# Performance work log

Hardware: AMD Instinct MI355X
Metric: run time of the kernel (lower is better)

Reference implementation:

```python
import jax, jax.numpy as jnp
import numpy as np

N = 100000
E = 800000
HID = 128
HEADS = 4
HD = HID // HEADS  # 32
EPS_SOFTMAX = 1e-16
LN_EPS = 1e-5


def setup_inputs() -> dict:
    key = jax.random.key(0)
    ks = jax.random.split(key, 12)
    s = 1.0 / np.sqrt(HID)
    x = jax.random.normal(ks[0], (N, HID), dtype=jnp.float32)
    edge_index = jax.random.randint(ks[1], (2, E), 0, N, dtype=jnp.int64)
    Wq = jax.random.normal(ks[2], (HID, HID), dtype=jnp.float32) * s
    bq = jnp.zeros((HID,), jnp.float32)
    Wk = jax.random.normal(ks[3], (HID, HID), dtype=jnp.float32) * s
    bk = jnp.zeros((HID,), jnp.float32)
    Wv = jax.random.normal(ks[4], (HID, HID), dtype=jnp.float32) * s
    bv = jnp.zeros((HID,), jnp.float32)
    Ws = jax.random.normal(ks[5], (HID, HID), dtype=jnp.float32) * s
    bs = jnp.zeros((HID,), jnp.float32)
    gamma = jnp.ones((HID,), jnp.float32)
    beta = jnp.zeros((HID,), jnp.float32)
    return {"x": x, "edge_index": edge_index, "Wq": Wq, "bq": bq,
            "Wk": Wk, "bk": bk, "Wv": Wv, "bv": bv,
            "Ws": Ws, "bs": bs, "gamma": gamma, "beta": beta}


def _transformer_conv(x, edge_index, Wq, bq, Wk, bk, Wv, bv, Ws, bs, gamma, beta):
    src = edge_index[0]  # message source j
    dst = edge_index[1]  # message target i
    # Projections -> [N, HEADS, HD]
    q = (x @ Wq + bq).reshape(N, HEADS, HD)
    k = (x @ Wk + bk).reshape(N, HEADS, HD)
    v = (x @ Wv + bv).reshape(N, HEADS, HD)
    # Edge-wise attention logits [E, HEADS]
    alpha = jnp.einsum('ehd,ehd->eh', q[dst], k[src]) / np.sqrt(HD).astype(np.float32)
    # Segment (per-destination) softmax, numerically stable
    amax = jax.ops.segment_max(alpha, dst, num_segments=N)  # [N, HEADS]
    amax = jnp.where(jnp.isfinite(amax), amax, 0.0)
    ex = jnp.exp(alpha - amax[dst])
    denom = jax.ops.segment_sum(ex, dst, num_segments=N)
    alpha = ex / (denom[dst] + EPS_SOFTMAX)
    # Weighted scatter-add of values
    out = jax.ops.segment_sum(alpha[:, :, None] * v[src], dst, num_segments=N)
    out = out.reshape(N, HID)
    # Root/skip connection (PyG root_weight=True, concat=True)
    out = out + x @ Ws + bs
    # LayerNorm
    mu = jnp.mean(out, axis=-1, keepdims=True)
    var = jnp.mean(jnp.square(out - mu), axis=-1, keepdims=True)
    return (out - mu) * jax.lax.rsqrt(var + LN_EPS) * gamma + beta


def reference(x, edge_index, Wq, bq, Wk, bk, Wv, bv, Ws, bs, gamma, beta):
    return _transformer_conv(x, edge_index, Wq, bq, Wk, bk, Wv, bv, Ws, bs, gamma, beta)
```

## Files before the change

### kernel.cpp

```cpp
#include <hip/hip_runtime.h>
#include <math.h>

#define N_NODES 100000
#define N_EDGES 800000
#define HID 128
#define HEADS 4
#define HD 32

#define KSCALE_L2E 0.2550348554422384f

#define PROJ_BLOCKS 1563
#define FILL_BLOCKS 3125

typedef __attribute__((ext_vector_type(8))) short short8;
typedef __attribute__((ext_vector_type(4))) float f32x4;
typedef _Float16 h2 __attribute__((ext_vector_type(2)));
typedef __fp16 hf2 __attribute__((ext_vector_type(2)));

__device__ __forceinline__ unsigned int f2bf(float f) {
    unsigned int u = __float_as_uint(f);
    u += 0x7FFFu + ((u >> 16) & 1u);
    return (u >> 16) & 0xFFFFu;
}
__device__ __forceinline__ h2 u2h(unsigned int u) { return __builtin_bit_cast(h2, u); }
__device__ __forceinline__ unsigned int h2u(h2 h) { return __builtin_bit_cast(unsigned int, h); }
__device__ __forceinline__ unsigned int h2u(hf2 h) { return __builtin_bit_cast(unsigned int, h); }

__global__ __launch_bounds__(256) void prep(
    const float* __restrict__ Wq, const float* __restrict__ Wk,
    const float* __restrict__ Wv, const float* __restrict__ Ws,
    uint4* __restrict__ wtbf, const int* __restrict__ ei,
    int* __restrict__ deg)
{
    const int b = blockIdx.x;
    if (b < 32) {
        int idx = b * 256 + threadIdx.x;
        int m = idx >> 11, n = (idx >> 4) & 127, kc = idx & 15;
        const float* W = (m == 0) ? Wq : (m == 1) ? Wk : (m == 2) ? Wv : Ws;
        unsigned int h[8];
        #pragma unroll
        for (int j = 0; j < 8; ++j) h[j] = f2bf(W[(kc * 8 + j) * HID + n]);
        uint4 o;
        o.x = h[0] | (h[1] << 16);
        o.y = h[2] | (h[3] << 16);
        o.z = h[4] | (h[5] << 16);
        o.w = h[6] | (h[7] << 16);
        wtbf[idx] = o;
    } else {
        int e = (b - 32) * 256 + threadIdx.x;
        if (e < N_EDGES) atomicAdd(&deg[ei[N_EDGES + e]], 1);
    }
}

__global__ __launch_bounds__(256) void scan_local(const int* __restrict__ deg,
                                                  int* __restrict__ rowptr,
                                                  int* __restrict__ bsum)
{
    __shared__ int wsums[4];
    const int b = blockIdx.x, t = threadIdx.x, lane = t & 63, wid = t >> 6;
    const int base = b * 2048 + t * 8;
    int v[8], s = 0;
    #pragma unroll
    for (int j = 0; j < 8; ++j) {
        int i = base + j;
        v[j] = (i < N_NODES) ? deg[i] : 0;
        s += v[j];
    }
    const int tsum = s;
    int x = tsum;
    #pragma unroll
    for (int off = 1; off < 64; off <<= 1) {
        int t2 = __shfl_up(x, off);
        if (lane >= off) x += t2;
    }
    if (lane == 63) wsums[wid] = x;
    __syncthreads();
    int wpre = 0;
    #pragma unroll
    for (int ww = 0; ww < 4; ++ww) { if (ww < wid) wpre += wsums[ww]; }
    int run = wpre + x - tsum;
    #pragma unroll
    for (int j = 0; j < 8; ++j) {
        int i = base + j;
        if (i < N_NODES) rowptr[i] = run;
        run += v[j];
    }
    if (t == 0) bsum[b] = wsums[0] + wsums[1] + wsums[2] + wsums[3];
}

__global__ __launch_bounds__(256) void add_off(int* __restrict__ rowptr,
                                               const int* __restrict__ bsum)
{
    __shared__ int offs;
    const int t = threadIdx.x;
    const int tgt = blockIdx.x >> 3;
    if (t < 64) {
        int v = (t < tgt) ? bsum[t] : 0;
        #pragma unroll
        for (int off = 1; off < 64; off <<= 1) v += __shfl_xor(v, off);
        if (t == 0) offs = v;
    }
    __syncthreads();
    int i = blockIdx.x * 256 + t;
    if (i < N_NODES) rowptr[i] += offs;
    if (blockIdx.x == 0 && t == 0) rowptr[N_NODES] = N_EDGES;
}

__global__ __launch_bounds__(256) void fill_proj(
    const int* __restrict__ ei, const int* __restrict__ rowptr,
    int* __restrict__ deg, int* __restrict__ csr_src,
    const float* __restrict__ x, const uint4* __restrict__ wtbf,
    const float* __restrict__ bq, const float* __restrict__ bk,
    const float* __restrict__ bv, const float* __restrict__ bs,
    unsigned short* __restrict__ Qh, unsigned short* __restrict__ KVh,
    unsigned short* __restrict__ Sh)
{
    __shared__ uint4 wt[2048];

    if (blockIdx.x >= PROJ_BLOCKS) {
        int e = (blockIdx.x - PROJ_BLOCKS) * 256 + threadIdx.x;
        if (e < N_EDGES) {
            int src = ei[e], dst = ei[N_EDGES + e];
            int old = atomicSub(&deg[dst], 1);
            csr_src[rowptr[dst] + old - 1] = src;
        }
        return;
    }

    const int rb   = blockIdx.x * 64;
    const int tid  = threadIdx.x;
    const int lane = tid & 63;
    const int w    = tid >> 6;
    const int r    = lane & 15;
    const int kg   = lane >> 4;

    const int grow = rb + w * 16 + r;
    short8 afr[4];
    #pragma unroll
    for (int s = 0; s < 4; ++s) {
        float4 a = make_float4(0.f, 0.f, 0.f, 0.f);
        float4 b = make_float4(0.f, 0.f, 0.f, 0.f);
        if (grow < N_NODES) {
            const float4* p = (const float4*)(x + (size_t)grow * HID + (s * 4 + kg) * 8);
            a = p[0]; b = p[1];
        }
        uint4 o;
        o.x = f2bf(a.x) | (f2bf(a.y) << 16);
        o.y = f2bf(a.z) | (f2bf(a.w) << 16);
        o.z = f2bf(b.x) | (f2bf(b.y) << 16);
        o.w = f2bf(b.z) | (f2bf(b.w) << 16);
        afr[s] = *(short8*)&o;
    }

    #pragma unroll
    for (int m = 0; m < 4; ++m) {
        if (m > 0) __syncthreads();
        #pragma unroll
        for (int it = 0; it < 8; ++it) {
            int cid = it * 256 + tid;
            int kc = cid & 15, n = (cid >> 4) & 127;
            wt[(cid & ~15) | (kc ^ (n & 7))] = wtbf[m * 2048 + cid];
        }
        __syncthreads();

        const float* bias = (m == 0) ? bq : (m == 1) ? bk : (m == 2) ? bv : bs;
        #pragma unroll
        for (int nt = 0; nt < 8; ++nt) {
            const int nrow = nt * 16 + r;
            const uint4* wrow = wt + nrow * 16;
            f32x4 acc;
            acc[0]=0.f; acc[1]=0.f; acc[2]=0.f; acc[3]=0.f;
            #pragma unroll
            for (int s = 0; s < 4; ++s) {
                short8 bfr = *(const short8*)&wrow[(s * 4 + kg) ^ (nrow & 7)];
                acc = __builtin_amdgcn_mfma_f32_16x16x32_bf16(bfr, afr[s], acc, 0, 0, 0);
            }
            if (grow < N_NODES) {
                const int col = nt * 16 + kg * 4;
                float4 bi = *(const float4*)(bias + col);
                float vx = acc[0] + bi.x, vy = acc[1] + bi.y;
                float vz = acc[2] + bi.z, vw = acc[3] + bi.w;
                if (m == 1) { vx *= KSCALE_L2E; vy *= KSCALE_L2E;
                              vz *= KSCALE_L2E; vw *= KSCALE_L2E; }
                uint2 pk;
                pk.x = h2u(__builtin_amdgcn_cvt_pkrtz(vx, vy));
                pk.y = h2u(__builtin_amdgcn_cvt_pkrtz(vz, vw));
                unsigned short* dst =
                    (m == 0) ? (Qh + (size_t)grow * HID + col) :
                    (m == 1) ? (KVh + (size_t)grow * 256 + col) :
                    (m == 2) ? (KVh + (size_t)grow * 256 + 128 + col) :
                               (Sh + (size_t)grow * HID + col);
                *(uint2*)dst = pk;
            }
        }
    }
}

__global__ __launch_bounds__(256) void node_attn(
    const int* __restrict__ rowptr, const int* __restrict__ csr_src,
    const unsigned short* __restrict__ Qh, const unsigned short* __restrict__ KVh,
    const unsigned short* __restrict__ Sh,
    const float* __restrict__ gamma, const float* __restrict__ beta,
    float* __restrict__ out)
{
    const int tid  = threadIdx.x;
    const int lane = tid & 63;
    const int node = blockIdx.x * 4 + (tid >> 6);
    if (node >= N_NODES) return;

    const int l16 = lane & 15;
    const int es  = lane >> 4;
    const int j8  = l16 * 8;

    const int r0 = rowptr[node], r1 = rowptr[node + 1];

    uint4 qp = *(const uint4*)(Qh + (size_t)node * HID + j8);
    const h2 qh0 = u2h(qp.x), qh1 = u2h(qp.y), qh2 = u2h(qp.z), qh3 = u2h(qp.w);

    float den = 0.f;
    h2 ac0 = {0, 0}, ac1 = {0, 0}, ac2 = {0, 0}, ac3 = {0, 0};

    int pA = r0 + es;
    int pB = pA + 4;
    uint4 kA = {0,0,0,0}, vA = {0,0,0,0}, kB = {0,0,0,0}, vB = {0,0,0,0};
    if (pA < r1) {
        const unsigned short* base = KVh + (size_t)csr_src[pA] * 256;
        kA = *(const uint4*)(base + j8);
        vA = *(const uint4*)(base + 128 + j8);
    }
    if (pB < r1) {
        const unsigned short* base = KVh + (size_t)csr_src[pB] * 256;
        kB = *(const uint4*)(base + j8);
        vB = *(const uint4*)(base + 128 + j8);
    }

    for (int it = r0; it < r1; it += 4) {
        const int pn = pA + 8;
        uint4 kn = {0,0,0,0}, vn = {0,0,0,0};
        if (pn < r1) {
            const unsigned short* base = KVh + (size_t)csr_src[pn] * 256;
            kn = *(const uint4*)(base + j8);
            vn = *(const uint4*)(base + 128 + j8);
        }

        h2 d = qh0 * u2h(kA.x);
        d += qh1 * u2h(kA.y);
        d += qh2 * u2h(kA.z);
        d += qh3 * u2h(kA.w);
        float t = (float)d.x + (float)d.y;
        t += __shfl_xor(t, 1);
        t += __shfl_xor(t, 2);

        float e = (pA < r1) ? __builtin_amdgcn_exp2f(t) : 0.f;
        den += e;
        _Float16 eh = (_Float16)e;
        h2 e2 = {eh, eh};
        ac0 += e2 * u2h(vA.x);
        ac1 += e2 * u2h(vA.y);
        ac2 += e2 * u2h(vA.z);
        ac3 += e2 * u2h(vA.w);

        pA = pB; pB = pn;
        kA = kB; vA = vB; kB = kn; vB = vn;
    }

    #pragma unroll
    for (int msk = 16; msk <= 32; msk <<= 1) {
        den += __shfl_xor(den, msk);
        ac0 += u2h(__shfl_xor(h2u(ac0), msk));
        ac1 += u2h(__shfl_xor(h2u(ac1), msk));
        ac2 += u2h(__shfl_xor(h2u(ac2), msk));
        ac3 += u2h(__shfl_xor(h2u(ac3), msk));
    }

    float inv = 1.0f / (den + 1e-16f);
    uint4 sp = *(const uint4*)(Sh + (size_t)node * HID + j8);
    const h2 s0 = u2h(sp.x), s1 = u2h(sp.y), s2 = u2h(sp.z), s3 = u2h(sp.w);
    float o0 = (float)ac0.x * inv + (float)s0.x, o1 = (float)ac0.y * inv + (float)s0.y;
    float o2 = (float)ac1.x * inv + (float)s1.x, o3 = (float)ac1.y * inv + (float)s1.y;
    float o4 = (float)ac2.x * inv + (float)s2.x, o5 = (float)ac2.y * inv + (float)s2.y;
    float o6 = (float)ac3.x * inv + (float)s3.x, o7 = (float)ac3.y * inv + (float)s3.y;

    float sum = (o0 + o1) + (o2 + o3) + (o4 + o5) + (o6 + o7);
    float sq  = o0*o0 + o1*o1 + o2*o2 + o3*o3 + o4*o4 + o5*o5 + o6*o6 + o7*o7;
    #pragma unroll
    for (int off = 1; off < 16; off <<= 1) {
        sum += __shfl_xor(sum, off);
        sq  += __shfl_xor(sq, off);
    }
    float mean = sum * (1.0f / 128.0f);
    float var  = sq * (1.0f / 128.0f) - mean * mean;
    float rstd = rsqrtf(var + 1e-5f);

    if (es == 0) {
        float4 g0 = *(const float4*)(gamma + j8);
        float4 g1 = *(const float4*)(gamma + j8 + 4);
        float4 b0 = *(const float4*)(beta + j8);
        float4 b1 = *(const float4*)(beta + j8 + 4);
        float4 w0, w1;
        w0.x = (o0 - mean) * rstd * g0.x + b0.x;
        w0.y = (o1 - mean) * rstd * g0.y + b0.y;
        w0.z = (o2 - mean) * rstd * g0.z + b0.z;
        w0.w = (o3 - mean) * rstd * g0.w + b0.w;
        w1.x = (o4 - mean) * rstd * g1.x + b1.x;
        w1.y = (o5 - mean) * rstd * g1.y + b1.y;
        w1.z = (o6 - mean) * rstd * g1.z + b1.z;
        w1.w = (o7 - mean) * rstd * g1.w + b1.w;
        float* op = out + (size_t)node * HID + j8;
        *(float4*)op = w0;
        *(float4*)(op + 4) = w1;
    }
}

extern "C" void kernel_launch(void* const* d_in, const int* in_sizes, int n_in,
                              void* d_out, int out_size, void* d_ws, size_t ws_size,
                              hipStream_t stream) {
    const float* x  = (const float*)d_in[0];
    const int*   ei = (const int*)d_in[1];
    const float* Wq = (const float*)d_in[2];
    const float* bq = (const float*)d_in[3];
    const float* Wk = (const float*)d_in[4];
    const float* bk = (const float*)d_in[5];
    const float* Wv = (const float*)d_in[6];
    const float* bv = (const float*)d_in[7];
    const float* Ws = (const float*)d_in[8];
    const float* bs = (const float*)d_in[9];
    const float* gamma = (const float*)d_in[10];
    const float* beta  = (const float*)d_in[11];
    float* out = (float*)d_out;

    unsigned short* Qh  = (unsigned short*)d_ws;
    unsigned short* KVh = Qh + (size_t)N_NODES * HID;
    unsigned short* Sh  = KVh + (size_t)N_NODES * 256;
    uint4* wtbf  = (uint4*)(Sh + (size_t)N_NODES * HID);
    int* deg     = (int*)(wtbf + 4 * 128 * 16);
    int* rowptr  = deg + N_NODES;
    int* csr_src = rowptr + (N_NODES + 1);
    int* bsum    = csr_src + N_EDGES;

    hipMemsetAsync(deg, 0, N_NODES * sizeof(int), stream);

    const int eblk = (N_EDGES + 255) / 256;
    prep<<<32 + eblk, 256, 0, stream>>>(Wq, Wk, Wv, Ws, wtbf, ei, deg);

    const int nb = (N_NODES + 2047) / 2048;
    scan_local<<<nb, 256, 0, stream>>>(deg, rowptr, bsum);
    add_off<<<(N_NODES + 255) / 256, 256, 0, stream>>>(rowptr, bsum);

    fill_proj<<<PROJ_BLOCKS + FILL_BLOCKS, 256, 0, stream>>>(
        ei, rowptr, deg, csr_src, x, wtbf, bq, bk, bv, bs, Qh, KVh, Sh);

    node_attn<<<(N_NODES + 3) / 4, 256, 0, stream>>>(rowptr, csr_src, Qh, KVh, Sh,
                                                     gamma, beta, out);
}
```

Before: 204.7 us.

## Pre-swizzle weights into MFMA fragment order and stream from global, drop LDS

The prep kernel now writes bf16 weights already arranged in per-lane MFMA fragment order. The projection blocks then read each lane's fragment straight from global/L2 with a one-step register prefetch, instead of staging all weights through shared memory behind barriers. This removes the 32 KB LDS buffer and the per-matrix syncthreads, which may raise occupancy, at the cost of each wave re-reading the weights from cache. The workspace offset for deg is updated to match the new weight buffer size, which is the same number of elements.

Measured after the change: 206.1 us. About the same (+0.7%).

```diff
diff --git a/kernel.cpp b/kernel.cpp
--- a/kernel.cpp
+++ b/kernel.cpp
@@ -35,11 +35,18 @@
     const int b = blockIdx.x;
     if (b < 32) {
         int idx = b * 256 + threadIdx.x;
-        int m = idx >> 11, n = (idx >> 4) & 127, kc = idx & 15;
+        int lane = idx & 63;
+        int s    = (idx >> 6) & 3;
+        int nt   = (idx >> 8) & 7;
+        int m    = idx >> 11;
+        int r    = lane & 15;
+        int kg   = lane >> 4;
         const float* W = (m == 0) ? Wq : (m == 1) ? Wk : (m == 2) ? Wv : Ws;
+        const int n  = nt * 16 + r;
+        const int k0 = (s * 4 + kg) * 8;
         unsigned int h[8];
         #pragma unroll
-        for (int j = 0; j < 8; ++j) h[j] = f2bf(W[(kc * 8 + j) * HID + n]);
+        for (int j = 0; j < 8; ++j) h[j] = f2bf(W[(k0 + j) * HID + n]);
         uint4 o;
         o.x = h[0] | (h[1] << 16);
         o.y = h[2] | (h[3] << 16);
@@ -115,8 +122,6 @@
     unsigned short* __restrict__ Qh, unsigned short* __restrict__ KVh,
     unsigned short* __restrict__ Sh)
 {
-    __shared__ uint4 wt[2048];
-
     if (blockIdx.x >= PROJ_BLOCKS) {
         int e = (blockIdx.x - PROJ_BLOCKS) * 256 + threadIdx.x;
         if (e < N_EDGES) {
@@ -127,14 +132,13 @@
         return;
     }
 
-    const int rb   = blockIdx.x * 64;
     const int tid  = threadIdx.x;
     const int lane = tid & 63;
     const int w    = tid >> 6;
     const int r    = lane & 15;
     const int kg   = lane >> 4;
 
-    const int grow = rb + w * 16 + r;
+    const int grow = blockIdx.x * 64 + w * 16 + r;
     short8 afr[4];
     #pragma unroll
     for (int s = 0; s < 4; ++s) {
@@ -152,47 +156,46 @@
         afr[s] = *(short8*)&o;
     }
 
-    #pragma unroll
-    for (int m = 0; m < 4; ++m) {
-        if (m > 0) __syncthreads();
+    uint4 wc[4], wn[4];
+    #pragma unroll
+    for (int s = 0; s < 4; ++s) wc[s] = wtbf[s * 64 + lane];
+
+    #pragma unroll
+    for (int mi = 0; mi < 32; ++mi) {
+        if (mi < 31) {
+            #pragma unroll
+            for (int s = 0; s < 4; ++s)
+                wn[s] = wtbf[((mi + 1) * 4 + s) * 64 + lane];
+        }
+
+        f32x4 acc;
+        acc[0]=0.f; acc[1]=0.f; acc[2]=0.f; acc[3]=0.f;
         #pragma unroll
-        for (int it = 0; it < 8; ++it) {
-            int cid = it * 256 + tid;
-            int kc = cid & 15, n = (cid >> 4) & 127;
-            wt[(cid & ~15) | (kc ^ (n & 7))] = wtbf[m * 2048 + cid];
-        }
-        __syncthreads();
-
-        const float* bias = (m == 0) ? bq : (m == 1) ? bk : (m == 2) ? bv : bs;
+        for (int s = 0; s < 4; ++s)
+            acc = __builtin_amdgcn_mfma_f32_16x16x32_bf16(*(short8*)&wc[s], afr[s], acc, 0, 0, 0);
+
+        const int m = mi >> 3, nt = mi & 7;
+        if (grow < N_NODES) {
+            const float* bias = (m == 0) ? bq : (m == 1) ? bk : (m == 2) ? bv : bs;
+            const int col = nt * 16 + kg * 4;
+            float4 bi = *(const float4*)(bias + col);
+            float vx = acc[0] + bi.x, vy = acc[1] + bi.y;
+            float vz = acc[2] + bi.z, vw = acc[3] + bi.w;
+            if (m == 1) { vx *= KSCALE_L2E; vy *= KSCALE_L2E;
+                          vz *= KSCALE_L2E; vw *= KSCALE_L2E; }
+            uint2 pk;
+            pk.x = h2u(__builtin_amdgcn_cvt_pkrtz(vx, vy));
+            pk.y = h2u(__builtin_amdgcn_cvt_pkrtz(vz, vw));
+            unsigned short* dst =
+                (m == 0) ? (Qh + (size_t)grow * HID + col) :
+                (m == 1) ? (KVh + (size_t)grow * 256 + col) :
+                (m == 2) ? (KVh + (size_t)grow * 256 + 128 + col) :
+                           (Sh + (size_t)grow * HID + col);
+            *(uint2*)dst = pk;
+        }
+
         #pragma unroll
-        for (int nt = 0; nt < 8; ++nt) {
-            const int nrow = nt * 16 + r;
-            const uint4* wrow = wt + nrow * 16;
-            f32x4 acc;
-            acc[0]=0.f; acc[1]=0.f; acc[2]=0.f; acc[3]=0.f;
-            #pragma unroll
-            for (int s = 0; s < 4; ++s) {
-                short8 bfr = *(const short8*)&wrow[(s * 4 + kg) ^ (nrow & 7)];
-                acc = __builtin_amdgcn_mfma_f32_16x16x32_bf16(bfr, afr[s], acc, 0, 0, 0);
-            }
-            if (grow < N_NODES) {
-                const int col = nt * 16 + kg * 4;
-                float4 bi = *(const float4*)(bias + col);
-                float vx = acc[0] + bi.x, vy = acc[1] + bi.y;
-                float vz = acc[2] + bi.z, vw = acc[3] + bi.w;
-                if (m == 1) { vx *= KSCALE_L2E; vy *= KSCALE_L2E;
-                              vz *= KSCALE_L2E; vw *= KSCALE_L2E; }
-                uint2 pk;
-                pk.x = h2u(__builtin_amdgcn_cvt_pkrtz(vx, vy));
-                pk.y = h2u(__builtin_amdgcn_cvt_pkrtz(vz, vw));
-                unsigned short* dst =
-                    (m == 0) ? (Qh + (size_t)grow * HID + col) :
-                    (m == 1) ? (KVh + (size_t)grow * 256 + col) :
-                    (m == 2) ? (KVh + (size_t)grow * 256 + 128 + col) :
-                               (Sh + (size_t)grow * HID + col);
-                *(uint2*)dst = pk;
-            }
-        }
+        for (int s = 0; s < 4; ++s) wc[s] = wn[s];
     }
 }
 
@@ -333,7 +336,7 @@
     unsigned short* KVh = Qh + (size_t)N_NODES * HID;
     unsigned short* Sh  = KVh + (size_t)N_NODES * 256;
     uint4* wtbf  = (uint4*)(Sh + (size_t)N_NODES * HID);
-    int* deg     = (int*)(wtbf + 4 * 128 * 16);
+    int* deg     = (int*)(wtbf + 4 * 8 * 4 * 64);
     int* rowptr  = deg + N_NODES;
     int* csr_src = rowptr + (N_NODES + 1);
     int* bsum    = csr_src + N_EDGES;
```
